# Kernel optimization log

Hardware: AMD Instinct MI355X
Metric: run time of the kernel (lower is better)

## Reference

```python
import jax, jax.numpy as jnp
from jax import lax
import numpy as np

N_VOX = 50000
B = 2
D, H, W = 8, 160, 160
CIN = 16
G = 3
K = 27
CHANS = [(16, 16), (16, 32), (32, 64), (64, 64), (64, 128)]
NAMES = ['in', 'e1', 'e2', 'e3', 'out']


def setup_inputs() -> dict:
    key = jax.random.key(0)
    ks = jax.random.split(key, 16)
    rng = np.random.default_rng(0)
    # unique active cells -> deterministic scatter/gather rulebook
    lin = rng.choice(B * D * H * W, size=N_VOX, replace=False)
    bz = lin // (D * H * W)
    rem = lin % (D * H * W)
    zz = rem // (H * W)
    yy = (rem % (H * W)) // W
    xx = rem % W
    coors = jnp.asarray(np.stack([bz, zz, yy, xx], 1).astype(np.int32))
    inp = {
        'voxel_features': jax.random.normal(ks[0], (N_VOX, CIN), jnp.float32),
        'coors': coors,
        'batch_size': B,
    }
    i = 1
    for nm, (ci, co) in zip(NAMES, CHANS):
        k1, k2 = jax.random.split(ks[i]); i += 1
        inp['wb_' + nm] = jax.random.normal(k1, (K, ci, co), jnp.float32) * 0.05
        inp['ws_' + nm] = jax.random.normal(k2, (K, ci, G, co), jnp.float32) * 0.05
        inp['gm_' + nm] = jnp.ones((co,), jnp.float32)
        inp['bt_' + nm] = jnp.zeros((co,), jnp.float32)
    return inp


def _kan_block(feat, nbr, wb, ws, gm, bt, centers, inv_h):
    # submanifold KAN conv: gather -> (silu base + RBF spline basis) GEMM -> accumulate
    n = feat.shape[0]
    fp = jnp.concatenate([feat, jnp.zeros((1, feat.shape[1]), feat.dtype)], 0)  # pad row for out-of-grid

    def body(acc, kin):
        idx, wbk, wsk = kin
        x = fp[idx]                                   # [N, Cin] gathered neighbors
        base = jax.nn.silu(x) @ wbk                   # [N, Cout]
        bas = jnp.exp(-jnp.square((x[:, :, None] - centers) * inv_h))  # [N, Cin, G]
        spl = jnp.einsum('ncg,cgo->no', bas, wsk)     # [N, Cout]
        return acc + base + spl, None

    out0 = jnp.zeros((n, wb.shape[-1]), feat.dtype)
    out, _ = lax.scan(jax.checkpoint(body), out0, (nbr, wb, ws))
    # BatchNorm1d (train-mode batch stats) + ReLU
    mu = out.mean(0)
    var = out.var(0)
    out = (out - mu) * lax.rsqrt(var + 1e-3) * gm + bt
    return jax.nn.relu(out)


def _build_rulebook(coors, batch_size, n):
    grid = jnp.full((batch_size, D + 2, H + 2, W + 2), n, jnp.int32)
    grid = grid.at[coors[:, 0], coors[:, 1] + 1, coors[:, 2] + 1, coors[:, 3] + 1].set(
        jnp.arange(n, dtype=jnp.int32))
    offs = [(dz, dy, dx) for dz in (-1, 0, 1) for dy in (-1, 0, 1) for dx in (-1, 0, 1)]
    return jnp.stack([
        grid[coors[:, 0], coors[:, 1] + 1 + dz, coors[:, 2] + 1 + dy, coors[:, 3] + 1 + dx]
        for dz, dy, dx in offs])  # [27, N]


def reference(voxel_features, coors, batch_size,
              wb_in, ws_in, gm_in, bt_in,
              wb_e1, ws_e1, gm_e1, bt_e1,
              wb_e2, ws_e2, gm_e2, bt_e2,
              wb_e3, ws_e3, gm_e3, bt_e3,
              wb_out, ws_out, gm_out, bt_out):
    n = voxel_features.shape[0]
    nbr = _build_rulebook(coors, batch_size, n)
    centers = jnp.linspace(-1.0, 1.0, G)
    inv_h = (G - 1) / 2.0
    x = _kan_block(voxel_features, nbr, wb_in, ws_in, gm_in, bt_in, centers, inv_h)
    x = _kan_block(x, nbr, wb_e1, ws_e1, gm_e1, bt_e1, centers, inv_h)
    x = _kan_block(x, nbr, wb_e2, ws_e2, gm_e2, bt_e2, centers, inv_h)
    x = _kan_block(x, nbr, wb_e3, ws_e3, gm_e3, bt_e3, centers, inv_h)
    x = _kan_block(x, nbr, wb_out, ws_out, gm_out, bt_out, centers, inv_h)
    co = x.shape[1]
    dense = jnp.zeros((batch_size, D, H, W, co), x.dtype)
    dense = dense.at[coors[:, 0], coors[:, 1], coors[:, 2], coors[:, 3]].set(x)
    dense = dense.transpose(0, 4, 1, 2, 3)            # [B, C, D, H, W]
    return dense.reshape(batch_size, co * D, H, W)    # [B, C*D, H, W]
```

## Files before the change

kernel.cpp:

```cpp
#include <hip/hip_runtime.h>

#define N_VOX 50000
#define BATCH 2
#define DD 8
#define HH 160
#define WW 160
#define PD 10
#define PH 162
#define PW 162
#define KK 27
#define NCELL (BATCH*DD*HH*WW)
#define GRID_ELEMS (BATCH*PD*PH*PW)
#define OUT_ELEMS (BATCH*128*DD*HH*WW)

typedef __attribute__((ext_vector_type(8))) short short8v;
typedef __attribute__((ext_vector_type(4))) float float4v;

__device__ inline unsigned short f2bf(float f) {
    unsigned u = __float_as_uint(f);
    u += 0x7FFFu + ((u >> 16) & 1u);
    return (unsigned short)(u >> 16);
}

__device__ inline void gload_lds16(const void* g, void* l) {
    __builtin_amdgcn_global_load_lds(
        (const __attribute__((address_space(1))) void*)g,
        (__attribute__((address_space(3))) void*)l, 16, 0, 0);
}

__global__ void k_flags(const int* __restrict__ coors, int* __restrict__ flags) {
    int n = blockIdx.x * 256 + threadIdx.x;
    if (n >= N_VOX) return;
    int b = coors[n*4+0], z = coors[n*4+1], y = coors[n*4+2], x = coors[n*4+3];
    flags[((b*DD + z)*HH + y)*WW + x] = 1;
}

__global__ void k_scan1(const int* __restrict__ flags, int* __restrict__ scanout,
                        int* __restrict__ bsums) {
    __shared__ int s[256];
    int t = threadIdx.x, blk = blockIdx.x;
    int4 v = ((const int4*)(flags + blk*1024))[t];
    int tsum = v.x + v.y + v.z + v.w;
    s[t] = tsum; __syncthreads();
    for (int off = 1; off < 256; off <<= 1) {
        int x = (t >= off) ? s[t-off] : 0;
        __syncthreads(); s[t] += x; __syncthreads();
    }
    int excl = s[t] - tsum;
    int4 o; o.x = excl; o.y = excl + v.x; o.z = o.y + v.y; o.w = o.z + v.z;
    ((int4*)(scanout + blk*1024))[t] = o;
    if (t == 255) bsums[blk] = s[255];
}

__global__ void k_scan2(int* __restrict__ bsums) {
    __shared__ int s[512];
    int t = threadIdx.x;
    int orig = (t < 400) ? bsums[t] : 0;
    s[t] = orig; __syncthreads();
    for (int off = 1; off < 512; off <<= 1) {
        int x = (t >= off) ? s[t-off] : 0;
        __syncthreads(); s[t] += x; __syncthreads();
    }
    if (t < 400) bsums[t] = s[t] - orig;
}

__global__ void k_pos(const int* __restrict__ coors, const int* __restrict__ scanout,
                      const int* __restrict__ bsums, int* __restrict__ pos_of,
                      int* __restrict__ vox_at) {
    int n = blockIdx.x * 256 + threadIdx.x;
    if (n >= N_VOX) return;
    int b = coors[n*4+0], z = coors[n*4+1], y = coors[n*4+2], x = coors[n*4+3];
    int lin = ((b*DD + z)*HH + y)*WW + x;
    int pos = scanout[lin] + bsums[lin >> 10];
    pos_of[n] = pos;
    vox_at[pos] = n;
}

__global__ void k_gridP(const int* __restrict__ coors, const int* __restrict__ pos_of,
                        int* __restrict__ gridP) {
    int n = blockIdx.x * 256 + threadIdx.x;
    if (n >= N_VOX) return;
    int b = coors[n*4+0], z = coors[n*4+1], y = coors[n*4+2], x = coors[n*4+3];
    gridP[((b*PD + z+1)*PH + (y+1))*PW + (x+1)] = pos_of[n];
}

__global__ void k_nbrP(const int* __restrict__ coors, const int* __restrict__ vox_at,
                       const int* __restrict__ gridP, int* __restrict__ nbrP) {
    int i = blockIdx.x * 256 + threadIdx.x;
    if (i >= N_VOX) return;
    int n = vox_at[i];
    int b = coors[n*4+0], z = coors[n*4+1]+1, y = coors[n*4+2]+1, x = coors[n*4+3]+1;
    int k = 0;
    for (int dz = -1; dz <= 1; ++dz)
        for (int dy = -1; dy <= 1; ++dy)
            for (int dx = -1; dx <= 1; ++dx) {
                int g = gridP[((b*PD + z+dz)*PH + (y+dy))*PW + (x+dx)];
                nbrP[k*N_VOX + i] = (g >= 0) ? g : N_VOX;
                ++k;
            }
}

__global__ void k_phi0(const float* __restrict__ vf, const int* __restrict__ vox_at,
                       unsigned short* __restrict__ phi) {
    int e = blockIdx.x * 256 + threadIdx.x;
    if (e >= (N_VOX + 1) * 16) return;
    int i = e / 16, c = e % 16;
    float x = 0.f;
    if (i < N_VOX) x = vf[(size_t)vox_at[i] * 16 + c];
    float sig = 1.f / (1.f + __expf(-x));
    ushort4 p;
    p.x = f2bf(x * sig);
    p.y = f2bf(__expf(-(x + 1.f) * (x + 1.f)));
    p.z = f2bf(__expf(-x * x));
    p.w = f2bf(__expf(-(x - 1.f) * (x - 1.f)));
    *(ushort4*)&phi[(size_t)e * 4] = p;
}

struct WswzArgs {
    const float* wb[5];
    const float* ws[5];
    unsigned short* dst[5];
};
__global__ void k_wswz_all(WswzArgs a) {
    constexpr int off[6]   = {0, 27648, 82944, 304128, 746496, 1631232};
    constexpr int lgCI4[5] = {6, 6, 7, 8, 8};
    constexpr int lgCO[5]  = {4, 5, 6, 6, 7};
    int e = blockIdx.x * 256 + threadIdx.x;
    if (e >= off[5]) return;
    int L = 0;
    #pragma unroll
    for (int i = 1; i < 5; ++i) L += (e >= off[i]);
    int el = e - off[L];
    int CIN4 = 1 << lgCI4[L], COUT = 1 << lgCO[L], CIN = CIN4 >> 2;
    int j8   = el & 7;
    int rest = el >> 3;
    int o    = rest & (COUT - 1);
    int kb   = rest >> lgCO[L];
    int kabs = kb * 8 + j8;
    int k  = kabs >> lgCI4[L];
    int c4 = kabs & (CIN4 - 1);
    int c = c4 >> 2, jj = c4 & 3;
    float v = (jj == 0) ? a.wb[L][(k * CIN + c) * COUT + o]
                        : a.ws[L][((k * CIN + c) * 3 + (jj - 1)) * COUT + o];
    a.dst[L][el] = f2bf(v);
}

template<int CIN, int COUT, int NSPL>
__global__ __launch_bounds__(64, 2) void k_conv_mfma(
    const unsigned short* __restrict__ phi,
    const int*            __restrict__ nbrP,
    const unsigned short* __restrict__ Wsw,
    float*                __restrict__ pre,
    float*                __restrict__ sums)
{
    constexpr int CIN4   = CIN * 4;
    constexpr int BK     = 64;
    constexpr int SPK    = CIN4 / BK;
    constexpr int NSTAGE = KK * SPK;
    constexpr int COUTH  = COUT / NSPL;
    constexpr int NFW    = COUTH / 16;
    constexpr int WR     = 4;
    constexpr int NMB    = (N_VOX + 63) / 64;
    constexpr int NBLK   = NMB * NSPL;
    constexpr int PERX   = (NBLK + 7) / 8;

    int lb = blockIdx.x;
    int linear = (lb & 7) * PERX + (lb >> 3);
    if (linear >= NBLK) return;
    const int mb = linear / NSPL, h = linear % NSPL;

    const int lane = threadIdx.x & 63;
    const int l15 = lane & 15, q = lane >> 4;
    const int base = mb * 64;
    int vg[WR];
    #pragma unroll
    for (int rs = 0; rs < WR; ++rs) vg[rs] = base + rs * 16 + l15;
    const int ob = h * COUTH;

    const unsigned short* bp = Wsw + (size_t)(q * COUT + ob + l15) * 8;

    int rows[WR], rowsN[WR];
    short8v A0[2][WR], A1[2][WR];
    short8v B0[2][NFW], B1[2][NFW];

    auto loadB = [&](int sp, short8v (&Bb)[2][NFW]) {
        #pragma unroll
        for (int kk = 0; kk < 2; ++kk)
            #pragma unroll
            for (int nf = 0; nf < NFW; ++nf)
                Bb[kk][nf] = *(const short8v*)(bp +
                    ((size_t)(sp * 8 + kk * 4) * COUT + nf * 16) * 8);
    };
    auto loadA = [&](int sp, short8v (&Ab)[2][WR]) {
        if (sp % SPK == 0) {
            #pragma unroll
            for (int rs = 0; rs < WR; ++rs) rows[rs] = rowsN[rs];
        }
        const int c4s = (sp % SPK) * BK;
        #pragma unroll
        for (int rs = 0; rs < WR; ++rs) {
            const unsigned short* p = phi + (size_t)rows[rs] * CIN4 + c4s + q * 8;
            Ab[0][rs] = *(const short8v*)p;
            Ab[1][rs] = *(const short8v*)(p + 32);
        }
        if (sp % SPK == 0) {
            int k2 = sp / SPK + 1;
            if (k2 < KK) {
                #pragma unroll
                for (int rs = 0; rs < WR; ++rs)
                    rowsN[rs] = (vg[rs] < N_VOX) ? nbrP[k2 * N_VOX + vg[rs]] : N_VOX;
            }
        }
    };

    float4v acc[WR][NFW];
    #pragma unroll
    for (int rs = 0; rs < WR; ++rs)
        #pragma unroll
        for (int nf = 0; nf < NFW; ++nf)
            acc[rs][nf] = (float4v){0.f, 0.f, 0.f, 0.f};

    auto domfma = [&](const short8v (&Ab)[2][WR], const short8v (&Bb)[2][NFW]) {
        #pragma unroll
        for (int kk = 0; kk < 2; ++kk)
            #pragma unroll
            for (int nf = 0; nf < NFW; ++nf)
                #pragma unroll
                for (int rs = 0; rs < WR; ++rs)
                    acc[rs][nf] = __builtin_amdgcn_mfma_f32_16x16x32_bf16(
                        Ab[kk][rs], Bb[kk][nf], acc[rs][nf], 0, 0, 0);
    };

    #pragma unroll
    for (int rs = 0; rs < WR; ++rs) {
        rows[rs]  = (vg[rs] < N_VOX) ? nbrP[vg[rs]] : N_VOX;
        rowsN[rs] = (vg[rs] < N_VOX) ? nbrP[N_VOX + vg[rs]] : N_VOX;
    }
    loadB(0, B0);
    #pragma unroll
    for (int rs = 0; rs < WR; ++rs) {
        const unsigned short* p = phi + (size_t)rows[rs] * CIN4 + q * 8;
        A0[0][rs] = *(const short8v*)p;
        A0[1][rs] = *(const short8v*)(p + 32);
    }

    #define SLOT(T, Ac, Bc, An, Bn)                                   \
        if ((T) + 1 < NSTAGE) { loadB((T) + 1, Bn); loadA((T) + 1, An); } \
        __builtin_amdgcn_sched_barrier(0);                            \
        domfma(Ac, Bc);

    int s = 0;
    for (; s + 2 <= NSTAGE; s += 2) {
        SLOT(s + 0, A0, B0, A1, B1)
        SLOT(s + 1, A1, B1, A0, B0)
    }
    if constexpr (NSTAGE % 2 != 0) {
        domfma(A0, B0);
    }
    #undef SLOT

    #pragma unroll
    for (int rs = 0; rs < WR; ++rs)
        #pragma unroll
        for (int nf = 0; nf < NFW; ++nf)
            #pragma unroll
            for (int r = 0; r < 4; ++r) {
                int v = base + rs * 16 + q * 4 + r;
                if (v < N_VOX)
                    pre[(size_t)v * COUT + ob + nf * 16 + l15] = acc[rs][nf][r];
            }

    float* S = sums + (blockIdx.x & 7) * 256;
    #pragma unroll
    for (int nf = 0; nf < NFW; ++nf) {
        float s1 = 0.f, s2 = 0.f;
        #pragma unroll
        for (int rs = 0; rs < WR; ++rs)
            #pragma unroll
            for (int r = 0; r < 4; ++r) {
                int v = base + rs * 16 + q * 4 + r;
                if (v < N_VOX) {
                    float a = acc[rs][nf][r];
                    s1 += a; s2 += a * a;
                }
            }
        s1 += __shfl_xor(s1, 16); s1 += __shfl_xor(s1, 32);
        s2 += __shfl_xor(s2, 16); s2 += __shfl_xor(s2, 32);
        if (q == 0) {
            atomicAdd(&S[ob + nf * 16 + l15], s1);
            atomicAdd(&S[COUT + ob + nf * 16 + l15], s2);
        }
    }
}

template<int CIN, int COUT, int NSPL>
__global__ __launch_bounds__(512, 2) void k_conv_bsh(
    const unsigned short* __restrict__ phi,
    const int*            __restrict__ nbrP,
    const unsigned short* __restrict__ Wsw,
    float*                __restrict__ pre,
    float*                __restrict__ sums)
{
    constexpr int CIN4   = CIN * 4;
    constexpr int BK     = 64;
    constexpr int SPK    = CIN4 / BK;
    constexpr int NSTAGE = KK * SPK;
    constexpr int KB_G   = 8 * SPK;
    constexpr int COUTH  = COUT / NSPL;
    constexpr int NFW    = COUTH / 16;
    constexpr int WR     = 2;
    constexpr int NMB    = (N_VOX + 255) / 256;
    constexpr int NBLK   = NMB * NSPL;
    constexpr int PERX   = (NBLK + 7) / 8;
    constexpr int SI     = KB_G / 8;

    __shared__ short8v ldsB[2][KB_G][64];

    int lb = blockIdx.x;
    int linear = (lb & 7) * PERX + (lb >> 3);
    if (linear >= NBLK) return;
    const int mb = linear / NSPL, h = linear % NSPL;

    const int t = threadIdx.x, lane = t & 63, w = t >> 6;
    const int l15 = lane & 15, q = lane >> 4;
    const int base = mb * 256 + w * 32;
    int vg[WR];
    #pragma unroll
    for (int rs = 0; rs < WR; ++rs) vg[rs] = base + rs * 16 + l15;
    const int ob = h * COUTH;

    int rows[WR], rowsN[WR];
    short8v A0[2][WR], A1[2][WR];

    auto stage = [&](int g) {
        #pragma unroll
        for (int j = 0; j < SI; ++j) {
            const int m = w * SI + j;
            gload_lds16(Wsw + ((size_t)(g * KB_G + m) * COUT + ob + lane) * 8,
                        &ldsB[g & 1][m][0]);
        }
    };
    auto loadA = [&](int sp, short8v (&Ab)[2][WR]) {
        if (sp % SPK == 0) {
            #pragma unroll
            for (int rs = 0; rs < WR; ++rs) rows[rs] = rowsN[rs];
        }
        const int c4s = (sp % SPK) * BK;
        #pragma unroll
        for (int rs = 0; rs < WR; ++rs) {
            const unsigned short* p = phi + (size_t)rows[rs] * CIN4 + c4s + q * 8;
            Ab[0][rs] = *(const short8v*)p;
            Ab[1][rs] = *(const short8v*)(p + 32);
        }
        if (sp % SPK == 0) {
            int k2 = sp / SPK + 1;
            if (k2 < KK) {
                #pragma unroll
                for (int rs = 0; rs < WR; ++rs)
                    rowsN[rs] = (vg[rs] < N_VOX) ? nbrP[k2 * N_VOX + vg[rs]] : N_VOX;
            }
        }
    };

    float4v acc[WR][NFW];
    #pragma unroll
    for (int rs = 0; rs < WR; ++rs)
        #pragma unroll
        for (int nf = 0; nf < NFW; ++nf)
            acc[rs][nf] = (float4v){0.f, 0.f, 0.f, 0.f};

    stage(0);
    __builtin_amdgcn_sched_barrier(0);
    #pragma unroll
    for (int rs = 0; rs < WR; ++rs) {
        rows[rs]  = (vg[rs] < N_VOX) ? nbrP[vg[rs]] : N_VOX;
        rowsN[rs] = (vg[rs] < N_VOX) ? nbrP[N_VOX + vg[rs]] : N_VOX;
    }
    #pragma unroll
    for (int rs = 0; rs < WR; ++rs) {
        const unsigned short* p = phi + (size_t)rows[rs] * CIN4 + q * 8;
        A0[0][rs] = *(const short8v*)p;
        A0[1][rs] = *(const short8v*)(p + 32);
    }

    int sp = 0;
    #define SLOTB(SG, Ac, An)                                                 \
    {                                                                         \
        short8v bf[2][NFW];                                                   \
        _Pragma("unroll") for (int kk = 0; kk < 2; ++kk)                      \
        _Pragma("unroll") for (int nf = 0; nf < NFW; ++nf)                    \
            bf[kk][nf] = ldsB[g & 1][(SG) * 8 + kk * 4 + q][nf * 16 + l15];   \
        if (sp + 1 < NSTAGE) loadA(sp + 1, An);                               \
        __builtin_amdgcn_sched_barrier(0);                                    \
        _Pragma("unroll") for (int kk = 0; kk < 2; ++kk)                      \
        _Pragma("unroll") for (int nf = 0; nf < NFW; ++nf)                    \
        _Pragma("unroll") for (int rs = 0; rs < WR; ++rs)                     \
            acc[rs][nf] = __builtin_amdgcn_mfma_f32_16x16x32_bf16(            \
                Ac[kk][rs], bf[kk][nf], acc[rs][nf], 0, 0, 0);                \
        ++sp;                                                                 \
    }

    for (int g = 0; g < KK; ++g) {
        if (g == 0) {
            asm volatile("s_waitcnt vmcnt(8)" ::: "memory");
        } else if (g == KK - 1) {
            asm volatile("s_waitcnt vmcnt(%0)" :: "i"(4 * SPK) : "memory");
        } else {
            asm volatile("s_waitcnt vmcnt(%0)" :: "i"(4 * SPK + 2) : "memory");
        }
        __builtin_amdgcn_sched_barrier(0);
        __builtin_amdgcn_s_barrier();
        __builtin_amdgcn_sched_barrier(0);
        if (g + 1 < KK) stage(g + 1);
        __builtin_amdgcn_sched_barrier(0);
        SLOTB(0, A0, A1)
        SLOTB(1, A1, A0)
        if constexpr (SPK == 4) {
            SLOTB(2, A0, A1)
            SLOTB(3, A1, A0)
        }
    }
    #undef SLOTB

    #pragma unroll
    for (int rs = 0; rs < WR; ++rs)
        #pragma unroll
        for (int nf = 0; nf < NFW; ++nf)
            #pragma unroll
            for (int r = 0; r < 4; ++r) {
                int v = base + rs * 16 + q * 4 + r;
                if (v < N_VOX)
                    pre[(size_t)v * COUT + ob + nf * 16 + l15] = acc[rs][nf][r];
            }

    float* S = sums + (blockIdx.x & 7) * 256;
    #pragma unroll
    for (int nf = 0; nf < NFW; ++nf) {
        float s1 = 0.f, s2 = 0.f;
        #pragma unroll
        for (int rs = 0; rs < WR; ++rs)
            #pragma unroll
            for (int r = 0; r < 4; ++r) {
                int v = base + rs * 16 + q * 4 + r;
                if (v < N_VOX) {
                    float a = acc[rs][nf][r];
                    s1 += a; s2 += a * a;
                }
            }
        s1 += __shfl_xor(s1, 16); s1 += __shfl_xor(s1, 32);
        s2 += __shfl_xor(s2, 16); s2 += __shfl_xor(s2, 32);
        if (q == 0) {
            atomicAdd(&S[ob + nf * 16 + l15], s1);
            atomicAdd(&S[COUT + ob + nf * 16 + l15], s2);
        }
    }
}

template<int COUT>
__global__ void k_bnapply_phi(const float* __restrict__ pre, const float* __restrict__ sums,
                              const float* __restrict__ gm, const float* __restrict__ bt,
                              unsigned short* __restrict__ phi) {
    __shared__ float sc[COUT], sh[COUT];
    int t = threadIdx.x;
    if (t < COUT) {
        float s1 = 0.f, s2 = 0.f;
        #pragma unroll
        for (int xo = 0; xo < 8; ++xo) {
            s1 += sums[xo * 256 + t];
            s2 += sums[xo * 256 + COUT + t];
        }
        float mu  = s1 * (1.f / N_VOX);
        float var = s2 * (1.f / N_VOX) - mu*mu;
        float s = rsqrtf(var + 1e-3f) * gm[t];
        sc[t] = s;
        sh[t] = bt[t] - mu * s;
    }
    __syncthreads();
    int tot = (N_VOX + 1) * COUT;
    for (int e = blockIdx.x*256 + t; e < tot; e += gridDim.x*256) {
        int i = e / COUT, c = e % COUT;
        float x = 0.f;
        if (i < N_VOX) x = fmaxf(pre[(size_t)i*COUT + c] * sc[c] + sh[c], 0.f);
        float sig = 1.f / (1.f + __expf(-x));
        ushort4 p;
        p.x = f2bf(x * sig);
        p.y = f2bf(__expf(-(x + 1.f) * (x + 1.f)));
        p.z = f2bf(__expf(-x * x));
        p.w = f2bf(__expf(-(x - 1.f) * (x - 1.f)));
        *(ushort4*)&phi[(size_t)e * 4] = p;
    }
}

__global__ void k_bnfin(const float* __restrict__ sums, const float* __restrict__ gm,
                        const float* __restrict__ bt, float* __restrict__ scsh) {
    int t = threadIdx.x;
    float s1 = 0.f, s2 = 0.f;
    #pragma unroll
    for (int xo = 0; xo < 8; ++xo) {
        s1 += sums[xo * 256 + t];
        s2 += sums[xo * 256 + 128 + t];
    }
    float mu  = s1 * (1.f / N_VOX);
    float var = s2 * (1.f / N_VOX) - mu*mu;
    float s = rsqrtf(var + 1e-3f) * gm[t];
    scsh[t]       = s;
    scsh[128 + t] = bt[t] - mu * s;
}

__global__ void k_dense(const float* __restrict__ feat, const int* __restrict__ gridP,
                        const float* __restrict__ scsh, float* __restrict__ out) {
    int e4 = blockIdx.x*256 + threadIdx.x;
    if (e4 >= OUT_ELEMS/4) return;
    int e = e4 * 4;
    int x  = e % WW;
    int y  = (e / WW) % HH;
    int cz = (e / (WW*HH)) % (128*DD);
    int b  = e / (WW*HH*128*DD);
    int c = cz >> 3, z = cz & 7;
    float sc = scsh[c], sh = scsh[128 + c];
    const int* gp = &gridP[((b*PD + z+1)*PH + (y+1))*PW + (x+1)];
    int g0 = gp[0], g1 = gp[1], g2 = gp[2], g3 = gp[3];
    float4 o;
    o.x = (g0 >= 0) ? fmaxf(feat[(size_t)g0*128 + c] * sc + sh, 0.f) : 0.f;
    o.y = (g1 >= 0) ? fmaxf(feat[(size_t)g1*128 + c] * sc + sh, 0.f) : 0.f;
    o.z = (g2 >= 0) ? fmaxf(feat[(size_t)g2*128 + c] * sc + sh, 0.f) : 0.f;
    o.w = (g3 >= 0) ? fmaxf(feat[(size_t)g3*128 + c] * sc + sh, 0.f) : 0.f;
    *(float4*)&out[e] = o;
}

template<int CIN, int COUT, int NSPL>
static void run_block(const float* gm, const float* bt,
                      const int* nbrP, unsigned short* phi, const unsigned short* Wsw,
                      float* sums, float* pre, hipStream_t stream) {
    constexpr int NMB  = (N_VOX + 63) / 64;
    constexpr int NBLK = NMB * NSPL;
    constexpr int GRID = ((NBLK + 7) / 8) * 8;
    k_conv_mfma<CIN, COUT, NSPL><<<GRID, 64, 0, stream>>>(phi, nbrP, Wsw, pre, sums);
    k_bnapply_phi<COUT><<<512, 256, 0, stream>>>(pre, sums, gm, bt, phi);
}

template<int CIN, int COUT, int NSPL>
static void run_block_bsh(const float* gm, const float* bt,
                          const int* nbrP, unsigned short* phi, const unsigned short* Wsw,
                          float* sums, float* pre, bool last, hipStream_t stream) {
    constexpr int NMB  = (N_VOX + 255) / 256;
    constexpr int NBLK = NMB * NSPL;
    constexpr int GRID = ((NBLK + 7) / 8) * 8;
    k_conv_bsh<CIN, COUT, NSPL><<<GRID, 512, 0, stream>>>(phi, nbrP, Wsw, pre, sums);
    if (!last)
        k_bnapply_phi<COUT><<<512, 256, 0, stream>>>(pre, sums, gm, bt, phi);
}

extern "C" void kernel_launch(void* const* d_in, const int* in_sizes, int n_in,
                              void* d_out, int out_size, void* d_ws, size_t ws_size,
                              hipStream_t stream) {
    const float* vf    = (const float*)d_in[0];
    const int*   coors = (const int*)d_in[1];
    const float* wb[5] = {(const float*)d_in[3],  (const float*)d_in[7],
                          (const float*)d_in[11], (const float*)d_in[15],
                          (const float*)d_in[19]};
    const float* wsp[5]= {(const float*)d_in[4],  (const float*)d_in[8],
                          (const float*)d_in[12], (const float*)d_in[16],
                          (const float*)d_in[20]};
    const float* gm[5] = {(const float*)d_in[5],  (const float*)d_in[9],
                          (const float*)d_in[13], (const float*)d_in[17],
                          (const float*)d_in[21]};
    const float* bt[5] = {(const float*)d_in[6],  (const float*)d_in[10],
                          (const float*)d_in[14], (const float*)d_in[18],
                          (const float*)d_in[22]};

    char* p = (char*)d_ws;
    auto alloc = [&](size_t bytes) {
        char* r = p;
        p += (bytes + 255) & ~(size_t)255;
        return r;
    };
    int*            flags   = (int*)           alloc((size_t)NCELL * 4);
    int*            scanout = (int*)           alloc((size_t)NCELL * 4);
    int*            bsums   = (int*)           alloc(512 * 4);
    int*            pos_of  = (int*)           alloc((size_t)N_VOX * 4);
    int*            vox_at  = (int*)           alloc((size_t)N_VOX * 4);
    int*            gridP   = (int*)           alloc((size_t)GRID_ELEMS * 4);
    int*            nbrP    = (int*)           alloc((size_t)KK * N_VOX * 4);
    unsigned short* Wsw0    = (unsigned short*)alloc((size_t)KK * 64  * 16  * 2);
    unsigned short* Wsw1    = (unsigned short*)alloc((size_t)KK * 64  * 32  * 2);
    unsigned short* Wsw2    = (unsigned short*)alloc((size_t)KK * 128 * 64  * 2);
    unsigned short* Wsw3    = (unsigned short*)alloc((size_t)KK * 256 * 64  * 2);
    unsigned short* Wsw4    = (unsigned short*)alloc((size_t)KK * 256 * 128 * 2);
    unsigned short* phi     = (unsigned short*)alloc((size_t)(N_VOX + 1) * 256 * 2);
    float*          sumsAll = (float*)         alloc(5 * 8 * 256 * 4);
    float*          pre     = (float*)         alloc((size_t)N_VOX * 128 * 4);
    float*          scsh    = (float*)         alloc(256 * 4);

    hipMemsetAsync(flags, 0, (size_t)NCELL * 4, stream);
    hipMemsetAsync(gridP, 0xFF, (size_t)GRID_ELEMS * 4, stream);
    hipMemsetAsync(sumsAll, 0, 5 * 8 * 256 * 4, stream);

    WswzArgs wa;
    for (int i = 0; i < 5; ++i) { wa.wb[i] = wb[i]; wa.ws[i] = wsp[i]; }
    wa.dst[0] = Wsw0; wa.dst[1] = Wsw1; wa.dst[2] = Wsw2; wa.dst[3] = Wsw3; wa.dst[4] = Wsw4;
    k_wswz_all<<<(1631232 + 255) / 256, 256, 0, stream>>>(wa);

    k_flags<<<(N_VOX+255)/256, 256, 0, stream>>>(coors, flags);
    k_scan1<<<NCELL/1024, 256, 0, stream>>>(flags, scanout, bsums);
    k_scan2<<<1, 512, 0, stream>>>(bsums);
    k_pos  <<<(N_VOX+255)/256, 256, 0, stream>>>(coors, scanout, bsums, pos_of, vox_at);
    k_gridP<<<(N_VOX+255)/256, 256, 0, stream>>>(coors, pos_of, gridP);
    k_nbrP <<<(N_VOX+255)/256, 256, 0, stream>>>(coors, vox_at, gridP, nbrP);
    {
        int n = (N_VOX + 1) * 16;
        k_phi0<<<(n + 255) / 256, 256, 0, stream>>>(vf, vox_at, phi);
    }

    run_block<16, 16, 1>(gm[0], bt[0], nbrP, phi, Wsw0, sumsAll + 0*2048, pre, stream);
    run_block<16, 32, 1>(gm[1], bt[1], nbrP, phi, Wsw1, sumsAll + 1*2048, pre, stream);
    run_block_bsh<32, 64,  1>(gm[2], bt[2], nbrP, phi, Wsw2, sumsAll + 2*2048, pre, false, stream);
    run_block_bsh<64, 64,  1>(gm[3], bt[3], nbrP, phi, Wsw3, sumsAll + 3*2048, pre, false, stream);
    run_block_bsh<64, 128, 2>(gm[4], bt[4], nbrP, phi, Wsw4, sumsAll + 4*2048, pre, true,  stream);

    k_bnfin<<<1, 128, 0, stream>>>(sumsAll + 4*2048, gm[4], bt[4], scsh);
    k_dense<<<(OUT_ELEMS/4 + 255)/256, 256, 0, stream>>>(pre, gridP, scsh, (float*)d_out);
}
```

Measured before the change: 629.5 us.

## Fuse position, grid scatter and first-layer basis into one kernel; raise conv occupancy

The position kernel now also writes the padded grid entry and computes the SiLU/RBF basis for the first layer directly at the sorted position. This removes two launches and the pos_of buffer. The pad row is filled by one extra thread using the basis values of zero. Separately, the launch bound of the big-shape conv kernel is raised from 2 to 4 blocks per SM. That may force register spills, and the fused per-thread loop writes strided, uncoalesced phi entries.

```diff
diff --git a/kernel.cpp b/kernel.cpp
--- a/kernel.cpp
+++ b/kernel.cpp
@@ -64,24 +64,39 @@
     if (t < 400) bsums[t] = s[t] - orig;
 }
 
-__global__ void k_pos(const int* __restrict__ coors, const int* __restrict__ scanout,
-                      const int* __restrict__ bsums, int* __restrict__ pos_of,
-                      int* __restrict__ vox_at) {
+__global__ void k_pos(const float* __restrict__ vf, const int* __restrict__ coors,
+                      const int* __restrict__ scanout, const int* __restrict__ bsums,
+                      int* __restrict__ vox_at, int* __restrict__ gridP,
+                      unsigned short* __restrict__ phi) {
     int n = blockIdx.x * 256 + threadIdx.x;
-    if (n >= N_VOX) return;
+    if (n > N_VOX) return;
+    if (n == N_VOX) {
+        ushort4 p;
+        p.x = f2bf(0.f);
+        p.y = f2bf(__expf(-1.f));
+        p.z = f2bf(1.f);
+        p.w = f2bf(__expf(-1.f));
+        #pragma unroll
+        for (int c = 0; c < 16; ++c)
+            *(ushort4*)&phi[((size_t)N_VOX * 16 + c) * 4] = p;
+        return;
+    }
     int b = coors[n*4+0], z = coors[n*4+1], y = coors[n*4+2], x = coors[n*4+3];
     int lin = ((b*DD + z)*HH + y)*WW + x;
     int pos = scanout[lin] + bsums[lin >> 10];
-    pos_of[n] = pos;
     vox_at[pos] = n;
-}
-
-__global__ void k_gridP(const int* __restrict__ coors, const int* __restrict__ pos_of,
-                        int* __restrict__ gridP) {
-    int n = blockIdx.x * 256 + threadIdx.x;
-    if (n >= N_VOX) return;
-    int b = coors[n*4+0], z = coors[n*4+1], y = coors[n*4+2], x = coors[n*4+3];
-    gridP[((b*PD + z+1)*PH + (y+1))*PW + (x+1)] = pos_of[n];
+    gridP[((b*PD + z+1)*PH + (y+1))*PW + (x+1)] = pos;
+    #pragma unroll
+    for (int c = 0; c < 16; ++c) {
+        float xv = vf[(size_t)n * 16 + c];
+        float sig = 1.f / (1.f + __expf(-xv));
+        ushort4 p;
+        p.x = f2bf(xv * sig);
+        p.y = f2bf(__expf(-(xv + 1.f) * (xv + 1.f)));
+        p.z = f2bf(__expf(-xv * xv));
+        p.w = f2bf(__expf(-(xv - 1.f) * (xv - 1.f)));
+        *(ushort4*)&phi[((size_t)pos * 16 + c) * 4] = p;
+    }
 }
 
 __global__ void k_nbrP(const int* __restrict__ coors, const int* __restrict__ vox_at,
@@ -98,22 +113,6 @@
                 nbrP[k*N_VOX + i] = (g >= 0) ? g : N_VOX;
                 ++k;
             }
-}
-
-__global__ void k_phi0(const float* __restrict__ vf, const int* __restrict__ vox_at,
-                       unsigned short* __restrict__ phi) {
-    int e = blockIdx.x * 256 + threadIdx.x;
-    if (e >= (N_VOX + 1) * 16) return;
-    int i = e / 16, c = e % 16;
-    float x = 0.f;
-    if (i < N_VOX) x = vf[(size_t)vox_at[i] * 16 + c];
-    float sig = 1.f / (1.f + __expf(-x));
-    ushort4 p;
-    p.x = f2bf(x * sig);
-    p.y = f2bf(__expf(-(x + 1.f) * (x + 1.f)));
-    p.z = f2bf(__expf(-x * x));
-    p.w = f2bf(__expf(-(x - 1.f) * (x - 1.f)));
-    *(ushort4*)&phi[(size_t)e * 4] = p;
 }
 
 struct WswzArgs {
@@ -294,7 +293,7 @@
 }
 
 template<int CIN, int COUT, int NSPL>
-__global__ __launch_bounds__(512, 2) void k_conv_bsh(
+__global__ __launch_bounds__(512, 4) void k_conv_bsh(
     const unsigned short* __restrict__ phi,
     const int*            __restrict__ nbrP,
     const unsigned short* __restrict__ Wsw,
@@ -578,7 +577,6 @@
     int*            flags   = (int*)           alloc((size_t)NCELL * 4);
     int*            scanout = (int*)           alloc((size_t)NCELL * 4);
     int*            bsums   = (int*)           alloc(512 * 4);
-    int*            pos_of  = (int*)           alloc((size_t)N_VOX * 4);
     int*            vox_at  = (int*)           alloc((size_t)N_VOX * 4);
     int*            gridP   = (int*)           alloc((size_t)GRID_ELEMS * 4);
     int*            nbrP    = (int*)           alloc((size_t)KK * N_VOX * 4);
@@ -604,13 +602,9 @@
     k_flags<<<(N_VOX+255)/256, 256, 0, stream>>>(coors, flags);
     k_scan1<<<NCELL/1024, 256, 0, stream>>>(flags, scanout, bsums);
     k_scan2<<<1, 512, 0, stream>>>(bsums);
-    k_pos  <<<(N_VOX+255)/256, 256, 0, stream>>>(coors, scanout, bsums, pos_of, vox_at);
-    k_gridP<<<(N_VOX+255)/256, 256, 0, stream>>>(coors, pos_of, gridP);
+    k_pos  <<<(N_VOX+1+255)/256, 256, 0, stream>>>(vf, coors, scanout, bsums,
+                                                   vox_at, gridP, phi);
     k_nbrP <<<(N_VOX+255)/256, 256, 0, stream>>>(coors, vox_at, gridP, nbrP);
-    {
-        int n = (N_VOX + 1) * 16;
-        k_phi0<<<(n + 255) / 256, 256, 0, stream>>>(vf, vox_at, phi);
-    }
 
     run_block<16, 16, 1>(gm[0], bt[0], nbrP, phi, Wsw0, sumsAll + 0*2048, pre, stream);
     run_block<16, 32, 1>(gm[1], bt[1], nbrP, phi, Wsw1, sumsAll + 1*2048, pre, stream);
```

Measured after the change: 614.7 us, median of 2. 2.4% less time.
